# Optimization experiments

Hardware: AMD Instinct MI355X
Metric: run time of the kernel (lower is better)

Reference implementation:

```python
import jax, jax.numpy as jnp
from jax import lax
import numpy as np

B = 2
N_PER = 12000
TIMES = 16
C_IN = 4
# sparse_shape = grid_size[::-1] + [1,0,0], grid_size=[160,160,40]
S1 = (41, 160, 160)
S2 = (21, 80, 80)   # conv2: k3 s2 p1
S3 = (11, 40, 40)   # conv3: k3 s2 p1
S4 = (5, 20, 20)    # conv4: k3 s2 p(0,1,1)
SOUT = (2, 20, 20)  # conv_out: k(3,1,1) s(2,1,1) p0
# per-BN-layer channel counts, flattened into gamma/beta vectors
CH = [16, 16, 32, 32, 32, 64, 64, 64, 64, 64, 64, 128]
OFF = np.concatenate([[0], np.cumsum(CH)]).tolist()


def _downsample_coords(coords, in_shape, k, s, p):
    # spconv SparseConv3d output index rule: output j active iff some active
    # input x satisfies j*s - p <= x <= j*s - p + k - 1 within bounds.
    out_shape = np.array([(in_shape[i] + 2 * p[i] - k[i]) // s[i] + 1 for i in range(3)])
    b, xs = coords[:, :1], coords[:, 1:]
    s_arr = np.array(s)
    cand = []
    for o0 in range(k[0]):
        for o1 in range(k[1]):
            for o2 in range(k[2]):
                j = xs + np.array([p[0] - o0, p[1] - o1, p[2] - o2])
                ok = np.all(j % s_arr == 0, axis=1)
                jj = j // s_arr
                ok &= np.all((jj >= 0) & (jj < out_shape), axis=1)
                cand.append(np.concatenate([b[ok], jj[ok]], axis=1))
    return np.unique(np.concatenate(cand, axis=0), axis=0).astype(np.int32)


def _make_coords():
    rng = np.random.default_rng(0)
    ncell = S1[0] * S1[1] * S1[2]
    per = []
    for b in range(B):
        flat = rng.choice(ncell, size=N_PER, replace=False)
        z, y, x = np.unravel_index(flat, S1)
        per.append(np.stack([np.full(N_PER, b), z, y, x], axis=1))
    c1 = np.concatenate(per, axis=0).astype(np.int32)
    c2 = _downsample_coords(c1, S1, (3, 3, 3), (2, 2, 2), (1, 1, 1))
    c3 = _downsample_coords(c2, S2, (3, 3, 3), (2, 2, 2), (1, 1, 1))
    c4 = _downsample_coords(c3, S3, (3, 3, 3), (2, 2, 2), (0, 1, 1))
    c5 = _downsample_coords(c4, S4, (3, 1, 1), (2, 1, 1), (0, 0, 0))
    return c1, c2, c3, c4, c5


def _w(key, shape):
    fan_in = shape[0] * shape[1] * shape[2] * shape[3]
    return jax.random.normal(key, shape, jnp.float32) * np.float32(np.sqrt(2.0 / fan_in))


def setup_inputs():
    c1, c2, c3, c4, c5 = _make_coords()
    ks = jax.random.split(jax.random.key(0), 16)
    t = TIMES
    return {
        "voxel_features": jax.random.normal(ks[0], (c1.shape[0], C_IN), jnp.float32),
        "w_in": _w(ks[1], (3, 3, 3, C_IN, t)),
        "w1": _w(ks[2], (3, 3, 3, t, t)),
        "w2_0": _w(ks[3], (3, 3, 3, t, 2 * t)),
        "w2_1": _w(ks[4], (3, 3, 3, 2 * t, 2 * t)),
        "w2_2": _w(ks[5], (3, 3, 3, 2 * t, 2 * t)),
        "w3_0": _w(ks[6], (3, 3, 3, 2 * t, 4 * t)),
        "w3_1": _w(ks[7], (3, 3, 3, 4 * t, 4 * t)),
        "w3_2": _w(ks[8], (3, 3, 3, 4 * t, 4 * t)),
        "w4_0": _w(ks[9], (3, 3, 3, 4 * t, 4 * t)),
        "w4_1": _w(ks[10], (3, 3, 3, 4 * t, 4 * t)),
        "w4_2": _w(ks[11], (3, 3, 3, 4 * t, 4 * t)),
        "w_out": _w(ks[12], (3, 1, 1, 4 * t, 8 * t)),
        "gamma": 1.0 + 0.1 * jax.random.normal(ks[13], (sum(CH),), jnp.float32),
        "beta": 0.1 * jax.random.normal(ks[14], (sum(CH),), jnp.float32),
        "coords1": jnp.asarray(c1), "coords2": jnp.asarray(c2),
        "coords3": jnp.asarray(c3), "coords4": jnp.asarray(c4),
        "coords_out": jnp.asarray(c5),
    }


def _sp_conv(feats, in_coords, w, in_shape, out_coords, stride, padding):
    # spconv's rulebook gather->matmul->scatter over active sites computes the
    # same values as a dense conv on a zero-filled grid, read back only at the
    # active output coordinates (subm: out_coords == in_coords).
    dense = jnp.zeros((B,) + in_shape + (feats.shape[1],), feats.dtype)
    dense = dense.at[in_coords[:, 0], in_coords[:, 1], in_coords[:, 2], in_coords[:, 3]].set(feats)
    out = lax.conv_general_dilated(dense, w, window_strides=stride,
                                   padding=[(p, p) for p in padding],
                                   dimension_numbers=("NDHWC", "DHWIO", "NDHWC"))
    return out[out_coords[:, 0], out_coords[:, 1], out_coords[:, 2], out_coords[:, 3]]


def _bn_relu(x, g, b):
    # nn.BatchNorm1d(eps=1e-3) in training mode over the active voxels, + ReLU
    mu = jnp.mean(x, axis=0)
    var = jnp.mean(jnp.square(x - mu), axis=0)
    return jax.nn.relu((x - mu) * (g * lax.rsqrt(var + 1e-3)) + b)


def _forward(voxel_features, ws, gamma, beta, c1, c2, c3, c4, c5):
    layers = [
        (0, c1, S1, c1, (1, 1, 1), (1, 1, 1)),   # conv_input (subm, 4->16)
        (1, c1, S1, c1, (1, 1, 1), (1, 1, 1)),   # conv1 (subm)
        (2, c1, S1, c2, (2, 2, 2), (1, 1, 1)),   # conv2 spconv s2
        (3, c2, S2, c2, (1, 1, 1), (1, 1, 1)),
        (4, c2, S2, c2, (1, 1, 1), (1, 1, 1)),
        (5, c2, S2, c3, (2, 2, 2), (1, 1, 1)),   # conv3 spconv s2
        (6, c3, S3, c3, (1, 1, 1), (1, 1, 1)),
        (7, c3, S3, c3, (1, 1, 1), (1, 1, 1)),
        (8, c3, S3, c4, (2, 2, 2), (0, 1, 1)),   # conv4 spconv s2, pad (0,1,1)
        (9, c4, S4, c4, (1, 1, 1), (1, 1, 1)),
        (10, c4, S4, c4, (1, 1, 1), (1, 1, 1)),
        (11, c4, S4, c5, (2, 1, 1), (0, 0, 0)),  # conv_out k(3,1,1) s(2,1,1)
    ]
    x = voxel_features
    for i, ci, si, co, st, pd in layers:
        x = _sp_conv(x, ci, ws[i], si, co, st, pd)
        x = _bn_relu(x, gamma[OFF[i]:OFF[i + 1]], beta[OFF[i]:OFF[i + 1]])
    return x  # encoded_spconv_tensor features, [N_out, 8*times]


def reference(voxel_features, w_in, w1, w2_0, w2_1, w2_2, w3_0, w3_1, w3_2,
              w4_0, w4_1, w4_2, w_out, gamma, beta,
              coords1, coords2, coords3, coords4, coords_out):
    ws = [w_in, w1, w2_0, w2_1, w2_2, w3_0, w3_1, w3_2, w4_0, w4_1, w4_2, w_out]
    return _forward(voxel_features, ws, gamma, beta,
                    coords1, coords2, coords3, coords4, coords_out)
```

## Files before the change

### kernel.cpp

```cpp
#include <hip/hip_runtime.h>
#include <hip/hip_bf16.h>


typedef __attribute__((ext_vector_type(8))) short bf16x8;
typedef __attribute__((ext_vector_type(4))) short bf16x4s;
typedef __attribute__((ext_vector_type(4))) float f32x4;

typedef const __attribute__((address_space(1))) unsigned int* gas_ptr;
typedef __attribute__((address_space(3))) unsigned int* las_ptr;

__device__ __forceinline__ void dma16(const unsigned short* g, unsigned short* l) {
    __builtin_amdgcn_global_load_lds((gas_ptr)g, (las_ptr)l, 16, 0, 0);
}

__device__ __forceinline__ int xcd_swz(int wg, int nwg) {
    const int x = wg & 7, i = wg >> 3;
    const int q = nwg >> 3, r = nwg & 7;
    return (x < r ? x * (q + 1) : r * (q + 1) + (x - r) * q) + i;
}

__device__ inline unsigned short f2bf(float f) {
    unsigned u = __builtin_bit_cast(unsigned, f);
    u += 0x7FFFu + ((u >> 16) & 1u);
    return (unsigned short)(u >> 16);
}

struct ScatterArgs {
    const int* coords[4];
    int* grid[4];
    int n[4];
    int D[4], H[4], W[4];
};

__global__ __launch_bounds__(256) void scatter_grid_all(ScatterArgs a) {
    const int l = blockIdx.y;
    const int i = blockIdx.x * 256 + threadIdx.x;
    if (i >= a.n[l]) return;
    const int* c = a.coords[l] + 4 * i;
    a.grid[l][((c[0] * a.D[l] + c[1]) * a.H[l] + c[2]) * a.W[l] + c[3]] = i;
}

struct PrepArgs {
    const float* src[11];
    unsigned short* dst[11];
    int T[11], CIN[11], COUT[11], total[11];
};

__global__ __launch_bounds__(256) void prep_w_all(PrepArgs a) {
    const int l = blockIdx.y;
    const int i = blockIdx.x * 256 + threadIdx.x;
    if (i >= a.total[l]) return;
    const int COUT = a.COUT[l], CIN = a.CIN[l], T = a.T[l];
    const int co = i % COUT; const int r = i / COUT; const int ci = r % CIN; const int t = r / CIN;
    unsigned short v = (t < T) ? f2bf(a.src[l][i]) : (unsigned short)0;
    a.dst[l][((size_t)t * COUT + co) * CIN + ci] = v;
}

__global__ __launch_bounds__(256, 4) void sp_conv0(const float* __restrict__ fin,
                                                   const int* __restrict__ grid,
                                                   const int* __restrict__ oc, int n_out,
                                                   const float* __restrict__ w,
                                                   float* __restrict__ out,
                                                   int D, int H, int W) {
    const int c = threadIdx.x & 15;
    const int p = (blockIdx.x * 256 + threadIdx.x) >> 4;
    if (p >= n_out) return;
    const int b   = oc[4*p+0];
    const int iz0 = oc[4*p+1] - 1;
    const int iy0 = oc[4*p+2] - 1;
    const int ix0 = oc[4*p+3] - 1;
    const int* gb = grid + b * (D * H * W);
    float acc = 0.f;
    for (int kd = 0; kd < 3; ++kd) {
        const int iz = iz0 + kd;
        if ((unsigned)iz >= (unsigned)D) continue;
        for (int kh = 0; kh < 3; ++kh) {
            const int iy = iy0 + kh;
            if ((unsigned)iy >= (unsigned)H) continue;
            for (int kw = 0; kw < 3; ++kw) {
                const int ix = ix0 + kw;
                if ((unsigned)ix >= (unsigned)W) continue;
                const int idx = gb[(iz*H + iy)*W + ix];
                if (idx < 0) continue;
                const float4 v = *(const float4*)(fin + (size_t)idx * 4);
                const float* wp = w + (size_t)((kd*3 + kh)*3 + kw) * 64 + c;
                acc = fmaf(v.x, wp[0],  acc);
                acc = fmaf(v.y, wp[16], acc);
                acc = fmaf(v.z, wp[32], acc);
                acc = fmaf(v.w, wp[48], acc);
            }
        }
    }
    out[(size_t)p*16 + c] = acc;
}

template<int COUT>
__global__ __launch_bounds__(256, 4) void sp_conv_lds16(
    const unsigned short* __restrict__ fin, const int* __restrict__ grid,
    const int* __restrict__ oc, int n_out,
    const unsigned short* __restrict__ wt, float* __restrict__ out,
    float* __restrict__ stats,
    int D, int H, int W, int sz, int sy, int sx, int pz, int py, int px)
{
    constexpr int T  = 27;
    constexpr int BT = 4;
    constexpr int TP = 28;
    constexpr int NT = COUT/16;
    constexpr int NB = (COUT == 16) ? BT/2 : BT;

    __shared__ unsigned short Abuf[4*BT*16*16];
    __shared__ unsigned short Bbuf[BT*COUT*16];
    __shared__ float ls[2*COUT];

    const int l     = threadIdx.x & 63;
    const int w     = threadIdx.x >> 6;
    const int n     = l & 15;
    const int quad  = l >> 4;
    const int pbase = xcd_swz(blockIdx.x, gridDim.x) * 64 + w * 16;

    if (threadIdx.x < 2*COUT) ls[threadIdx.x] = 0.f;

    int idx[TP];
    if (quad == 0) {
        int pc = pbase + n;
        if (pc > n_out - 1) pc = n_out - 1;
        const int4 cc = ((const int4*)oc)[pc];
        const int* gb = grid + cc.x * (D * H * W);
        const int iz0 = cc.y * sz - pz;
        const int iy0 = cc.z * sy - py;
        const int ix0 = cc.w * sx - px;
#pragma unroll
        for (int tap = 0; tap < TP; ++tap) {
            const int te = tap < T ? tap : 0;
            const int kd = te/9, kr = te%9, kh = kr/3, kw = kr%3;
            const int iz = iz0 + kd, iy = iy0 + kh, ix = ix0 + kw;
            const bool ok = (tap < T) && (unsigned)iz < (unsigned)D &&
                            (unsigned)iy < (unsigned)H && (unsigned)ix < (unsigned)W;
            const int cz = iz < 0 ? 0 : (iz >= D ? D-1 : iz);
            const int cy = iy < 0 ? 0 : (iy >= H ? H-1 : iy);
            const int cx = ix < 0 ? 0 : (ix >= W ? W-1 : ix);
            const int g = gb[(cz*H + cy)*W + cx];
            idx[tap] = ok ? g : -1;
        }
    }

    f32x4 acc[NT];
#pragma unroll
    for (int t = 0; t < NT; ++t) acc[t] = (f32x4){0.f, 0.f, 0.f, 0.f};

    const int h  = l >> 5;
    const int m  = (l >> 1) & 15;
    const int ch = l & 1;

#pragma unroll
    for (int tb0 = 0; tb0 < TP; tb0 += BT) {
#pragma unroll
        for (int q = 0; q < BT/2; ++q) {
            const int v0 = __shfl(idx[tb0 + 2*q],     m);
            const int v1 = __shfl(idx[tb0 + 2*q + 1], m);
            const int row = h ? v1 : v0;
            const unsigned short* gp = fin + (ptrdiff_t)row*16 + ch*8;
            unsigned short* lp = Abuf + (w*BT + 2*q)*16*16;
            dma16(gp, lp);
        }
        for (int q = w; q < NB; q += 4) {
            if constexpr (COUT == 16) {
                const int tap = tb0 + 2*q + h;
                const int tw = tap < T ? tap : T;
                const unsigned short* gp = wt + ((size_t)tw*COUT + m)*16 + ch*8;
                unsigned short* lp = Bbuf + (2*q)*COUT*16;
                dma16(gp, lp);
            } else {
                const int tap = tb0 + q;
                const int tw = tap < T ? tap : T;
                const int r = l >> 1;
                const unsigned short* gp = wt + ((size_t)tw*COUT + r)*16 + ch*8;
                unsigned short* lp = Bbuf + q*COUT*16;
                dma16(gp, lp);
            }
        }
        __syncthreads();
#pragma unroll
        for (int jp = 0; jp < BT/2; ++jp) {
            const int ts = 2*jp + (quad >> 1);
            bf16x8 a = *(const bf16x8*)(Abuf + ((w*BT + ts)*16 + n)*16 + (quad & 1)*8);
#pragma unroll
            for (int t = 0; t < NT; ++t) {
                bf16x8 b = *(const bf16x8*)(Bbuf + (ts*COUT + t*16 + n)*16 + (quad & 1)*8);
                acc[t] = __builtin_amdgcn_mfma_f32_16x16x32_bf16(a, b, acc[t], 0, 0, 0);
            }
        }
        __syncthreads();
    }

#pragma unroll
    for (int t = 0; t < NT; ++t)
#pragma unroll
        for (int r = 0; r < 4; ++r) {
            const int p = pbase + quad*4 + r;
            if (p < n_out) out[(size_t)p * COUT + t*16 + n] = acc[t][r];
        }

#pragma unroll
    for (int t = 0; t < NT; ++t) {
        float s1 = 0.f, s2 = 0.f;
#pragma unroll
        for (int r = 0; r < 4; ++r) {
            const int p = pbase + quad*4 + r;
            if (p < n_out) { const float v = acc[t][r]; s1 += v; s2 += v*v; }
        }
        s1 += __shfl_xor(s1, 16); s2 += __shfl_xor(s2, 16);
        s1 += __shfl_xor(s1, 32); s2 += __shfl_xor(s2, 32);
        if (quad == 0) {
            atomicAdd(&ls[t*16 + n], s1);
            atomicAdd(&ls[COUT + t*16 + n], s2);
        }
    }
    __syncthreads();
    if (threadIdx.x < 2*COUT) atomicAdd(&stats[threadIdx.x], ls[threadIdx.x]);
}

template<int CIN, int COUT, int BT, int KD, int KH, int KW, int MB>
__global__ __launch_bounds__(256, MB) void sp_conv_lds(
    const unsigned short* __restrict__ fin, const int* __restrict__ grid,
    const int* __restrict__ oc, int n_out,
    const unsigned short* __restrict__ wt, float* __restrict__ out,
    float* __restrict__ stats,
    int D, int H, int W, int sz, int sy, int sx, int pz, int py, int px)
{
    constexpr int T    = KD*KH*KW;
    constexpr int TP   = ((T + BT - 1)/BT)*BT;
    constexpr int NT   = COUT/16;
    constexpr int S    = CIN/32;
    constexpr int LPR  = CIN/8;
    constexpr int RPD  = 64/LPR;
    constexpr int ADMA = 16/RPD;
    constexpr int BDMA = COUT/RPD;

    __shared__ unsigned short Abuf[4*BT*16*CIN];
    __shared__ unsigned short Bbuf[BT*COUT*CIN];
    __shared__ float ls[2*COUT];

    const int l     = threadIdx.x & 63;
    const int w     = threadIdx.x >> 6;
    const int n     = l & 15;
    const int quad  = l >> 4;
    const int pbase = xcd_swz(blockIdx.x, gridDim.x) * 64 + w * 16;

    if (threadIdx.x < 2*COUT) ls[threadIdx.x] = 0.f;

    int idx[TP];
    if (quad == 0) {
        int pc = pbase + n;
        if (pc > n_out - 1) pc = n_out - 1;
        const int4 cc = ((const int4*)oc)[pc];
        const int* gb = grid + cc.x * (D * H * W);
        const int iz0 = cc.y * sz - pz;
        const int iy0 = cc.z * sy - py;
        const int ix0 = cc.w * sx - px;
#pragma unroll
        for (int tap = 0; tap < TP; ++tap) {
            const int te = tap < T ? tap : 0;
            const int kd = te/(KH*KW), kr = te%(KH*KW), kh = kr/KW, kw = kr%KW;
            const int iz = iz0 + kd, iy = iy0 + kh, ix = ix0 + kw;
            const bool ok = (tap < T) && (unsigned)iz < (unsigned)D &&
                            (unsigned)iy < (unsigned)H && (unsigned)ix < (unsigned)W;
            const int cz = iz < 0 ? 0 : (iz >= D ? D-1 : iz);
            const int cy = iy < 0 ? 0 : (iy >= H ? H-1 : iy);
            const int cx = ix < 0 ? 0 : (ix >= W ? W-1 : ix);
            const int g = gb[(cz*H + cy)*W + cx];
            idx[tap] = ok ? g : -1;
        }
    }

    f32x4 acc[NT];
#pragma unroll
    for (int t = 0; t < NT; ++t) acc[t] = (f32x4){0.f, 0.f, 0.f, 0.f};

#pragma unroll
    for (int tb0 = 0; tb0 < TP; tb0 += BT) {
#pragma unroll
        for (int j = 0; j < BT; ++j) {
#pragma unroll
            for (int d = 0; d < ADMA; ++d) {
                const int m  = d*RPD + l/LPR;
                const int i0 = __shfl(idx[tb0+j], m);
                const int slot = (l % LPR) ^ (m % LPR);
                const unsigned short* gp = fin + (ptrdiff_t)i0*CIN + slot*8;
                unsigned short* lp = Abuf + ((w*BT + j)*16 + d*RPD)*CIN;
                dma16(gp, lp);
            }
        }
        for (int q = w; q < BT*BDMA; q += 4) {
            const int j = q / BDMA, d = q % BDMA;
            const int t = tb0 + j;
            const int tw = t < T ? t : T;
            const int r  = d*RPD + l/LPR;
            const int slot = (l % LPR) ^ (r % LPR);
            const unsigned short* gp = wt + ((size_t)tw*COUT + r)*CIN + slot*8;
            unsigned short* lp = Bbuf + (j*COUT + d*RPD)*CIN;
            dma16(gp, lp);
        }
        __syncthreads();
#pragma unroll
        for (int j = 0; j < BT; ++j) {
            const unsigned short* Aw = Abuf + (w*BT + j)*16*CIN;
            const unsigned short* Bw = Bbuf + j*COUT*CIN;
#pragma unroll
            for (int s = 0; s < S; ++s) {
                const int c = s*4 + quad;
                bf16x8 a = *(const bf16x8*)(Aw + n*CIN + ((c ^ (n % LPR)) * 8));
#pragma unroll
                for (int t = 0; t < NT; ++t) {
                    const int r = t*16 + n;
                    bf16x8 b = *(const bf16x8*)(Bw + r*CIN + ((c ^ (r % LPR)) * 8));
                    acc[t] = __builtin_amdgcn_mfma_f32_16x16x32_bf16(a, b, acc[t], 0, 0, 0);
                }
            }
        }
        __syncthreads();
    }

#pragma unroll
    for (int t = 0; t < NT; ++t)
#pragma unroll
        for (int r = 0; r < 4; ++r) {
            const int p = pbase + quad*4 + r;
            if (p < n_out) out[(size_t)p * COUT + t*16 + n] = acc[t][r];
        }

#pragma unroll
    for (int t = 0; t < NT; ++t) {
        float s1 = 0.f, s2 = 0.f;
#pragma unroll
        for (int r = 0; r < 4; ++r) {
            const int p = pbase + quad*4 + r;
            if (p < n_out) { const float v = acc[t][r]; s1 += v; s2 += v*v; }
        }
        s1 += __shfl_xor(s1, 16); s2 += __shfl_xor(s2, 16);
        s1 += __shfl_xor(s1, 32); s2 += __shfl_xor(s2, 32);
        if (quad == 0) {
            atomicAdd(&ls[t*16 + n], s1);
            atomicAdd(&ls[COUT + t*16 + n], s2);
        }
    }
    __syncthreads();
    if (threadIdx.x < 2*COUT) atomicAdd(&stats[threadIdx.x], ls[threadIdx.x]);
}

template<int C>
__global__ __launch_bounds__(256) void reduce_stats(const float* __restrict__ x, int nn,
                                                    float* __restrict__ stats)
{
    constexpr int R = 256 / C;
    __shared__ float s1[256];
    __shared__ float s2[256];
    const int c = threadIdx.x % C;
    const int r = threadIdx.x / C;
    float a1 = 0.f, a2 = 0.f;
    for (int i = blockIdx.x * R + r; i < nn; i += R * gridDim.x) {
        float v = x[(size_t)i*C + c];
        a1 += v;
        a2 += v * v;
    }
    s1[threadIdx.x] = a1;
    s2[threadIdx.x] = a2;
    __syncthreads();
    for (int off = 128; off >= C; off >>= 1) {
        if (threadIdx.x < off) {
            s1[threadIdx.x] += s1[threadIdx.x + off];
            s2[threadIdx.x] += s2[threadIdx.x + off];
        }
        __syncthreads();
    }
    if (threadIdx.x < C) {
        atomicAdd(&stats[c],     s1[threadIdx.x]);
        atomicAdd(&stats[C + c], s2[threadIdx.x]);
    }
}

__device__ inline void stv4(float* p, float4 v) { *(float4*)p = v; }
__device__ inline void stv4(unsigned short* p, float4 v) {
    bf16x4s o;
    o.x = (short)f2bf(v.x); o.y = (short)f2bf(v.y);
    o.z = (short)f2bf(v.z); o.w = (short)f2bf(v.w);
    *(bf16x4s*)p = o;
}

template<int C, typename OUT>
__global__ __launch_bounds__(256) void bn_relu_apply(const float* __restrict__ x,
                                                     OUT* __restrict__ y, int nn,
                                                     const float* __restrict__ stats,
                                                     const float* __restrict__ gamma,
                                                     const float* __restrict__ beta)
{
    const size_t q = (size_t)blockIdx.x * blockDim.x + threadIdx.x;
    if (q >= (size_t)nn * (C/4)) return;
    const int c = (int)(q % (size_t)(C/4)) * 4;
    const float inv_n = 1.f / (float)nn;
    const float4 xv = *(const float4*)(x + q*4);
    const float4 s1 = *(const float4*)(stats + c);
    const float4 s2 = *(const float4*)(stats + C + c);
    const float4 gm = *(const float4*)(gamma + c);
    const float4 bt = *(const float4*)(beta + c);
    float4 o;
    { float mu=s1.x*inv_n, var=s2.x*inv_n-mu*mu, g=gm.x*rsqrtf(var+1e-3f);
      float v=(xv.x-mu)*g+bt.x; o.x = v>0.f? v:0.f; }
    { float mu=s1.y*inv_n, var=s2.y*inv_n-mu*mu, g=gm.y*rsqrtf(var+1e-3f);
      float v=(xv.y-mu)*g+bt.y; o.y = v>0.f? v:0.f; }
    { float mu=s1.z*inv_n, var=s2.z*inv_n-mu*mu, g=gm.z*rsqrtf(var+1e-3f);
      float v=(xv.z-mu)*g+bt.z; o.z = v>0.f? v:0.f; }
    { float mu=s1.w*inv_n, var=s2.w*inv_n-mu*mu, g=gm.w*rsqrtf(var+1e-3f);
      float v=(xv.w-mu)*g+bt.w; o.w = v>0.f? v:0.f; }
    stv4(y + q*4, o);
}

extern "C" void kernel_launch(void* const* d_in, const int* in_sizes, int n_in,
                              void* d_out, int out_size, void* d_ws, size_t ws_size,
                              hipStream_t stream) {
    const float* WPTR[12] = {
        (const float*)d_in[1], (const float*)d_in[2], (const float*)d_in[3],
        (const float*)d_in[4], (const float*)d_in[5], (const float*)d_in[6],
        (const float*)d_in[7], (const float*)d_in[8], (const float*)d_in[9],
        (const float*)d_in[10], (const float*)d_in[11], (const float*)d_in[12] };
    const float* vf    = (const float*)d_in[0];
    const float* gamma = (const float*)d_in[13];
    const float* beta  = (const float*)d_in[14];
    const int* c1 = (const int*)d_in[15];
    const int* c2 = (const int*)d_in[16];
    const int* c3 = (const int*)d_in[17];
    const int* c4 = (const int*)d_in[18];
    const int* c5 = (const int*)d_in[19];
    const int N1 = in_sizes[15] / 4;
    const int N2 = in_sizes[16] / 4;
    const int N3 = in_sizes[17] / 4;
    const int N4 = in_sizes[18] / 4;
    const int N5 = in_sizes[19] / 4;

    static const int LT[12]  = {27,27,27,27,27,27,27,27,27,27,27,3};
    static const int LCI[12] = {4,16,16,32,32,32,64,64,64,64,64,64};
    static const int LCO[12] = {16,16,32,32,32,64,64,64,64,64,64,128};

    const size_t G1 = (size_t)2*41*160*160;
    const size_t G2 = (size_t)2*21*80*80;
    const size_t G3 = (size_t)2*11*40*40;
    const size_t G4 = (size_t)2*5*20*20;
    int* grid1 = (int*)d_ws;
    int* grid2 = grid1 + G1;
    int* grid3 = grid2 + G2;
    int* grid4 = grid3 + G3;
    float* stats = (float*)(grid4 + G4);

    size_t maxE = (size_t)N1*16;
    if ((size_t)N2*32  > maxE) maxE = (size_t)N2*32;
    if ((size_t)N3*64  > maxE) maxE = (size_t)N3*64;
    if ((size_t)N4*64  > maxE) maxE = (size_t)N4*64;
    if ((size_t)N5*128 > maxE) maxE = (size_t)N5*128;
    maxE = (maxE + 7) & ~(size_t)7;

    float* raw = stats + 12*256;
    unsigned short* padA = (unsigned short*)(raw + maxE);
    unsigned short* fA   = padA + 128;
    unsigned short* padB = fA + maxE;
    unsigned short* fB   = padB + 128;
    unsigned short* wtb  = fB + maxE;
    size_t wtoff[12];
    {
        size_t o = 0;
        for (int i = 1; i < 12; ++i) {
            wtoff[i] = o;
            o += (size_t)(LT[i] + 1) * LCI[i] * LCO[i];
        }
    }

    hipMemsetAsync(grid1, 0xFF, (G1+G2+G3+G4)*sizeof(int), stream);
    hipMemsetAsync(stats, 0, 12*256*sizeof(float), stream);
    hipMemsetAsync(padA, 0, 128*sizeof(unsigned short), stream);
    hipMemsetAsync(padB, 0, 128*sizeof(unsigned short), stream);

    {
        ScatterArgs sa;
        sa.coords[0]=c1; sa.coords[1]=c2; sa.coords[2]=c3; sa.coords[3]=c4;
        sa.grid[0]=grid1; sa.grid[1]=grid2; sa.grid[2]=grid3; sa.grid[3]=grid4;
        sa.n[0]=N1; sa.n[1]=N2; sa.n[2]=N3; sa.n[3]=N4;
        sa.D[0]=41; sa.H[0]=160; sa.W[0]=160;
        sa.D[1]=21; sa.H[1]= 80; sa.W[1]= 80;
        sa.D[2]=11; sa.H[2]= 40; sa.W[2]= 40;
        sa.D[3]= 5; sa.H[3]= 20; sa.W[3]= 20;
        int mx = N1; if (N2>mx) mx=N2; if (N3>mx) mx=N3; if (N4>mx) mx=N4;
        dim3 g((mx + 255)/256, 4);
        scatter_grid_all<<<g, 256, 0, stream>>>(sa);
    }
    {
        PrepArgs pa;
        int mx = 0;
        for (int i = 1; i < 12; ++i) {
            pa.src[i-1] = WPTR[i];
            pa.dst[i-1] = wtb + wtoff[i];
            pa.T[i-1] = LT[i]; pa.CIN[i-1] = LCI[i]; pa.COUT[i-1] = LCO[i];
            pa.total[i-1] = (LT[i]+1)*LCI[i]*LCO[i];
            if (pa.total[i-1] > mx) mx = pa.total[i-1];
        }
        dim3 g((mx + 255)/256, 11);
        prep_w_all<<<g, 256, 0, stream>>>(pa);
    }

    enum { GOFF_0 = 0, GOFF_1 = 16, GOFF_2 = 32, GOFF_3 = 64, GOFF_4 = 96, GOFF_5 = 128,
           GOFF_6 = 192, GOFF_7 = 256, GOFF_8 = 320, GOFF_9 = 384, GOFF_10 = 448, GOFF_11 = 512 };

#define APPLY(i, COUT, NP, FOUT_T, FOUT) \
    bn_relu_apply<COUT, FOUT_T><<<(((size_t)(NP)*(COUT)/4) + 255)/256, 256, 0, stream>>>( \
        raw, FOUT, NP, stats + (i)*256, gamma + GOFF_##i, beta + GOFF_##i);

    sp_conv0<<<((size_t)N1*16 + 255)/256, 256, 0, stream>>>(vf, grid1, c1, N1, WPTR[0], raw, 41,160,160);
    { int rb = (N1 + 15)/16; if (rb > 240) rb = 240;
      reduce_stats<16><<<rb, 256, 0, stream>>>(raw, N1, stats + 0*256); }
    APPLY(0, 16, N1, unsigned short, fA);

#define CONVS(i, COUT, FIN, GRD, OC, NP, D,H,W, SZ,SY,SX, PZ,PY,PX) \
    sp_conv_lds16<COUT><<<((NP)+63)/64, 256, 0, stream>>>( \
        FIN, GRD, OC, NP, wtb + wtoff[i], raw, stats + (i)*256, D,H,W, SZ,SY,SX, PZ,PY,PX);

#define CONVL(i, CIN, COUT, BT, MB, KD,KH,KW, FIN, GRD, OC, NP, D,H,W, SZ,SY,SX, PZ,PY,PX) \
    sp_conv_lds<CIN,COUT,BT,KD,KH,KW,MB><<<((NP)+63)/64, 256, 0, stream>>>( \
        FIN, GRD, OC, NP, wtb + wtoff[i], raw, stats + (i)*256, D,H,W, SZ,SY,SX, PZ,PY,PX);

    CONVS( 1, 16,       fA, grid1, c1, N1, 41,160,160, 1,1,1, 1,1,1); APPLY( 1, 16, N1, unsigned short, fB);
    CONVS( 2, 32,       fB, grid1, c2, N2, 41,160,160, 2,2,2, 1,1,1); APPLY( 2, 32, N2, unsigned short, fA);
    CONVL ( 3, 32, 32, 7, 3, 3,3,3, fA, grid2, c2, N2, 21, 80, 80, 1,1,1, 1,1,1); APPLY( 3, 32, N2, unsigned short, fB);
    CONVL ( 4, 32, 32, 7, 3, 3,3,3, fB, grid2, c2, N2, 21, 80, 80, 1,1,1, 1,1,1); APPLY( 4, 32, N2, unsigned short, fA);
    CONVL ( 5, 32, 64, 5, 3, 3,3,3, fA, grid2, c3, N3, 21, 80, 80, 2,2,2, 1,1,1); APPLY( 5, 64, N3, unsigned short, fB);
    CONVL ( 6, 64, 64, 3, 3, 3,3,3, fB, grid3, c3, N3, 11, 40, 40, 1,1,1, 1,1,1); APPLY( 6, 64, N3, unsigned short, fA);
    CONVL ( 7, 64, 64, 3, 3, 3,3,3, fA, grid3, c3, N3, 11, 40, 40, 1,1,1, 1,1,1); APPLY( 7, 64, N3, unsigned short, fB);
    CONVL ( 8, 64, 64, 3, 3, 3,3,3, fB, grid3, c4, N4, 11, 40, 40, 2,2,2, 0,1,1); APPLY( 8, 64, N4, unsigned short, fA);
    CONVL ( 9, 64, 64, 3, 3, 3,3,3, fA, grid4, c4, N4,  5, 20, 20, 1,1,1, 1,1,1); APPLY( 9, 64, N4, unsigned short, fB);
    CONVL (10, 64, 64, 3, 3, 3,3,3, fB, grid4, c4, N4,  5, 20, 20, 1,1,1, 1,1,1); APPLY(10, 64, N4, unsigned short, fA);
    CONVL (11, 64,128, 1, 2, 3,1,1, fA, grid4, c5, N5,  5, 20, 20, 2,1,1, 0,0,0); APPLY(11, 128, N5, float, (float*)d_out);
#undef CONVS
#undef CONVL
#undef APPLY
}
```

Baseline: 416.3 us.

## Add 128-row sparse conv kernel sharing weight tiles across four waves

```diff
diff --git a/kernel.cpp b/kernel.cpp
--- a/kernel.cpp
+++ b/kernel.cpp
@@ -348,6 +348,147 @@
     if (threadIdx.x < 2*COUT) atomicAdd(&stats[threadIdx.x], ls[threadIdx.x]);
 }
 
+template<int CIN, int COUT, int BT, int MB>
+__global__ __launch_bounds__(256, MB) void sp_conv_big(
+    const unsigned short* __restrict__ fin, const int* __restrict__ grid,
+    const int* __restrict__ oc, int n_out,
+    const unsigned short* __restrict__ wt, float* __restrict__ out,
+    float* __restrict__ stats,
+    int D, int H, int W, int sz, int sy, int sx, int pz, int py, int px)
+{
+    constexpr int T    = 27;
+    constexpr int TP   = 28;
+    constexpr int MT   = 2;
+    constexpr int NT   = COUT/16;
+    constexpr int S    = CIN/32;
+    constexpr int LPR  = CIN/8;
+    constexpr int RPD  = 64/LPR;
+    constexpr int ADMA = 32/RPD;
+    constexpr int BDMA = COUT/RPD;
+
+    __shared__ unsigned short Abuf[4*BT*32*CIN];
+    __shared__ unsigned short Bbuf[BT*COUT*CIN];
+    __shared__ float ls[2*COUT];
+
+    const int l     = threadIdx.x & 63;
+    const int w     = threadIdx.x >> 6;
+    const int n     = l & 15;
+    const int quad  = l >> 4;
+    const int wbase = xcd_swz(blockIdx.x, gridDim.x) * 128 + w * 32;
+
+    if (threadIdx.x < 2*COUT) ls[threadIdx.x] = 0.f;
+
+    int idx[TP];
+    {
+        int pc = wbase + (l & 31);
+        if (pc > n_out - 1) pc = n_out - 1;
+        const int4 cc = ((const int4*)oc)[pc];
+        const int* gb = grid + cc.x * (D * H * W);
+        const int iz0 = cc.y * sz - pz;
+        const int iy0 = cc.z * sy - py;
+        const int ix0 = cc.w * sx - px;
+#pragma unroll
+        for (int tap = 0; tap < TP; ++tap) {
+            const int te = tap < T ? tap : 0;
+            const int kd = te/9, kr = te%9, kh = kr/3, kw = kr%3;
+            const int iz = iz0 + kd, iy = iy0 + kh, ix = ix0 + kw;
+            const bool ok = (tap < T) && (unsigned)iz < (unsigned)D &&
+                            (unsigned)iy < (unsigned)H && (unsigned)ix < (unsigned)W;
+            const int cz = iz < 0 ? 0 : (iz >= D ? D-1 : iz);
+            const int cy = iy < 0 ? 0 : (iy >= H ? H-1 : iy);
+            const int cx = ix < 0 ? 0 : (ix >= W ? W-1 : ix);
+            const int g = gb[(cz*H + cy)*W + cx];
+            idx[tap] = ok ? g : -1;
+        }
+    }
+
+    f32x4 acc[MT][NT];
+#pragma unroll
+    for (int mt = 0; mt < MT; ++mt)
+#pragma unroll
+        for (int t = 0; t < NT; ++t) acc[mt][t] = (f32x4){0.f, 0.f, 0.f, 0.f};
+
+#pragma unroll
+    for (int tb0 = 0; tb0 < TP; tb0 += BT) {
+#pragma unroll
+        for (int j = 0; j < BT; ++j) {
+#pragma unroll
+            for (int d = 0; d < ADMA; ++d) {
+                const int r  = d*RPD + l/LPR;
+                const int i0 = __shfl(idx[tb0+j], r);
+                const int slot = (l % LPR) ^ (r % LPR);
+                const unsigned short* gp = fin + (ptrdiff_t)i0*CIN + slot*8;
+                unsigned short* lp = Abuf + ((w*BT + j)*32 + d*RPD)*CIN;
+                dma16(gp, lp);
+            }
+        }
+        for (int q = w; q < BT*BDMA; q += 4) {
+            const int j = q / BDMA, d = q % BDMA;
+            const int t = tb0 + j;
+            const int tw = t < T ? t : T;
+            const int r  = d*RPD + l/LPR;
+            const int slot = (l % LPR) ^ (r % LPR);
+            const unsigned short* gp = wt + ((size_t)tw*COUT + r)*CIN + slot*8;
+            unsigned short* lp = Bbuf + (j*COUT + d*RPD)*CIN;
+            dma16(gp, lp);
+        }
+        __syncthreads();
+#pragma unroll
+        for (int j = 0; j < BT; ++j) {
+            const unsigned short* Aw = Abuf + (w*BT + j)*32*CIN;
+            const unsigned short* Bw = Bbuf + j*COUT*CIN;
+#pragma unroll
+            for (int s = 0; s < S; ++s) {
+                const int c = s*4 + quad;
+                bf16x8 bfr[NT];
+#pragma unroll
+                for (int t = 0; t < NT; ++t) {
+                    const int r = t*16 + n;
+                    bfr[t] = *(const bf16x8*)(Bw + r*CIN + ((c ^ (r % LPR)) * 8));
+                }
+#pragma unroll
+                for (int mt = 0; mt < MT; ++mt) {
+                    bf16x8 a = *(const bf16x8*)(Aw + (mt*16 + n)*CIN + ((c ^ (n % LPR)) * 8));
+#pragma unroll
+                    for (int t = 0; t < NT; ++t)
+                        acc[mt][t] = __builtin_amdgcn_mfma_f32_16x16x32_bf16(a, bfr[t], acc[mt][t], 0, 0, 0);
+                }
+            }
+        }
+        __syncthreads();
+    }
+
+#pragma unroll
+    for (int mt = 0; mt < MT; ++mt)
+#pragma unroll
+        for (int t = 0; t < NT; ++t)
+#pragma unroll
+            for (int r = 0; r < 4; ++r) {
+                const int p = wbase + mt*16 + quad*4 + r;
+                if (p < n_out) out[(size_t)p * COUT + t*16 + n] = acc[mt][t][r];
+            }
+
+#pragma unroll
+    for (int t = 0; t < NT; ++t) {
+        float s1 = 0.f, s2 = 0.f;
+#pragma unroll
+        for (int mt = 0; mt < MT; ++mt)
+#pragma unroll
+            for (int r = 0; r < 4; ++r) {
+                const int p = wbase + mt*16 + quad*4 + r;
+                if (p < n_out) { const float v = acc[mt][t][r]; s1 += v; s2 += v*v; }
+            }
+        s1 += __shfl_xor(s1, 16); s2 += __shfl_xor(s2, 16);
+        s1 += __shfl_xor(s1, 32); s2 += __shfl_xor(s2, 32);
+        if (quad == 0) {
+            atomicAdd(&ls[t*16 + n], s1);
+            atomicAdd(&ls[COUT + t*16 + n], s2);
+        }
+    }
+    __syncthreads();
+    if (threadIdx.x < 2*COUT) atomicAdd(&stats[threadIdx.x], ls[threadIdx.x]);
+}
+
 template<int C>
 __global__ __launch_bounds__(256) void reduce_stats(const float* __restrict__ x, int nn,
                                                     float* __restrict__ stats)
@@ -525,18 +666,23 @@
     sp_conv_lds<CIN,COUT,BT,KD,KH,KW,MB><<<((NP)+63)/64, 256, 0, stream>>>( \
         FIN, GRD, OC, NP, wtb + wtoff[i], raw, stats + (i)*256, D,H,W, SZ,SY,SX, PZ,PY,PX);
 
+#define CONVB(i, CIN, COUT, BT, MB, FIN, GRD, OC, NP, D,H,W, SZ,SY,SX, PZ,PY,PX) \
+    sp_conv_big<CIN,COUT,BT,MB><<<((NP)+127)/128, 256, 0, stream>>>( \
+        FIN, GRD, OC, NP, wtb + wtoff[i], raw, stats + (i)*256, D,H,W, SZ,SY,SX, PZ,PY,PX);
+
     CONVS( 1, 16,       fA, grid1, c1, N1, 41,160,160, 1,1,1, 1,1,1); APPLY( 1, 16, N1, unsigned short, fB);
     CONVS( 2, 32,       fB, grid1, c2, N2, 41,160,160, 2,2,2, 1,1,1); APPLY( 2, 32, N2, unsigned short, fA);
-    CONVL ( 3, 32, 32, 7, 3, 3,3,3, fA, grid2, c2, N2, 21, 80, 80, 1,1,1, 1,1,1); APPLY( 3, 32, N2, unsigned short, fB);
-    CONVL ( 4, 32, 32, 7, 3, 3,3,3, fB, grid2, c2, N2, 21, 80, 80, 1,1,1, 1,1,1); APPLY( 4, 32, N2, unsigned short, fA);
-    CONVL ( 5, 32, 64, 5, 3, 3,3,3, fA, grid2, c3, N3, 21, 80, 80, 2,2,2, 1,1,1); APPLY( 5, 64, N3, unsigned short, fB);
-    CONVL ( 6, 64, 64, 3, 3, 3,3,3, fB, grid3, c3, N3, 11, 40, 40, 1,1,1, 1,1,1); APPLY( 6, 64, N3, unsigned short, fA);
-    CONVL ( 7, 64, 64, 3, 3, 3,3,3, fA, grid3, c3, N3, 11, 40, 40, 1,1,1, 1,1,1); APPLY( 7, 64, N3, unsigned short, fB);
-    CONVL ( 8, 64, 64, 3, 3, 3,3,3, fB, grid3, c4, N4, 11, 40, 40, 2,2,2, 0,1,1); APPLY( 8, 64, N4, unsigned short, fA);
-    CONVL ( 9, 64, 64, 3, 3, 3,3,3, fA, grid4, c4, N4,  5, 20, 20, 1,1,1, 1,1,1); APPLY( 9, 64, N4, unsigned short, fB);
-    CONVL (10, 64, 64, 3, 3, 3,3,3, fB, grid4, c4, N4,  5, 20, 20, 1,1,1, 1,1,1); APPLY(10, 64, N4, unsigned short, fA);
-    CONVL (11, 64,128, 1, 2, 3,1,1, fA, grid4, c5, N5,  5, 20, 20, 2,1,1, 0,0,0); APPLY(11, 128, N5, float, (float*)d_out);
+    CONVB ( 3, 32, 32, 7, 2, fA, grid2, c2, N2, 21, 80, 80, 1,1,1, 1,1,1); APPLY( 3, 32, N2, unsigned short, fB);
+    CONVB ( 4, 32, 32, 7, 2, fB, grid2, c2, N2, 21, 80, 80, 1,1,1, 1,1,1); APPLY( 4, 32, N2, unsigned short, fA);
+    CONVB ( 5, 32, 64, 4, 3, fA, grid2, c3, N3, 21, 80, 80, 2,2,2, 1,1,1); APPLY( 5, 64, N3, unsigned short, fB);
+    CONVB ( 6, 64, 64, 3, 2, fB, grid3, c3, N3, 11, 40, 40, 1,1,1, 1,1,1); APPLY( 6, 64, N3, unsigned short, fA);
+    CONVB ( 7, 64, 64, 3, 2, fA, grid3, c3, N3, 11, 40, 40, 1,1,1, 1,1,1); APPLY( 7, 64, N3, unsigned short, fB);
+    CONVL ( 8, 64, 64, 9, 1, 3,3,3, fB, grid3, c4, N4, 11, 40, 40, 2,2,2, 0,1,1); APPLY( 8, 64, N4, unsigned short, fA);
+    CONVL ( 9, 64, 64, 9, 1, 3,3,3, fA, grid4, c4, N4,  5, 20, 20, 1,1,1, 1,1,1); APPLY( 9, 64, N4, unsigned short, fB);
+    CONVL (10, 64, 64, 9, 1, 3,3,3, fB, grid4, c4, N4,  5, 20, 20, 1,1,1, 1,1,1); APPLY(10, 64, N4, unsigned short, fA);
+    CONVL (11, 64,128, 3, 2, 3,1,1, fA, grid4, c5, N5,  5, 20, 20, 2,1,1, 0,0,0); APPLY(11, 128, N5, float, (float*)d_out);
 #undef CONVS
 #undef CONVL
+#undef CONVB
 #undef APPLY
 }
```

Measured after the change: 398.3 us. 4.3% less time.
